# Performance work log

Hardware: AMD Instinct MI355X
Metric: run time of the kernel (lower is better)

## Reference

```python
import jax, jax.numpy as jnp
import numpy as np

B, H, W, C, HEADS = 4, 64, 64, 512, 8
HD = C // HEADS
L = H * W
BIAS_LEVEL = 0.1
LN_EPS = 1e-5


def _ln(x, g, b):
    mu = jnp.mean(x, axis=-1, keepdims=True)
    var = jnp.var(x, axis=-1, keepdims=True)
    return (x - mu) * jax.lax.rsqrt(var + LN_EPS) * g + b


def setup_inputs() -> dict:
    key = jax.random.key(0)
    ks = jax.random.split(key, 16)
    s = 0.02
    return {
        "x": jax.random.normal(ks[0], (B, L, C), jnp.float32),
        "rpe": jax.random.normal(ks[1], (H, HEADS, W, W), jnp.float32),
        "qkv_w": jax.random.normal(ks[2], (3 * C, C), jnp.float32) * s,
        "proj_w": jax.random.normal(ks[3], (C, C), jnp.float32) * s,
        "proj_b": jnp.zeros((C,), jnp.float32),
        "norm1_w": jnp.ones((C,), jnp.float32),
        "norm1_b": jnp.zeros((C,), jnp.float32),
        "norm2_w": jnp.ones((C,), jnp.float32),
        "norm2_b": jnp.zeros((C,), jnp.float32),
        "fc1_w": jax.random.normal(ks[4], (4 * C, C), jnp.float32) * s,
        "fc1_b": jnp.zeros((4 * C,), jnp.float32),
        "fc2_w": jax.random.normal(ks[5], (C, 4 * C), jnp.float32) * s,
        "fc2_b": jnp.zeros((C,), jnp.float32),
    }


def reference(x, rpe, qkv_w, proj_w, proj_b, norm1_w, norm1_b, norm2_w, norm2_b,
              fc1_w, fc1_b, fc2_w, fc2_b):
    # --- qkv projection ---
    img = _ln(x, norm1_w, norm1_b)
    qkv = (img @ qkv_w.T).reshape(B, L, 3, C)
    q, k, v = qkv[:, :, 0], qkv[:, :, 1], qkv[:, :, 2]

    # idx=0 horizontal windows: each row of the HxW grid is a window of len W.
    def to_win(t):  # (B, L, C) -> (B*H, heads, W, hd)
        return t.reshape(B * H, W, HEADS, HD).transpose(0, 2, 1, 3)

    qw, kw, vw = to_win(q), to_win(k), to_win(v)

    # attention scores + relative position bias (RPE tiled over batch)
    attn = jnp.einsum('whqd,whkd->whqk', qw, kw)
    attn = attn + BIAS_LEVEL * jnp.tile(rpe, (B, 1, 1, 1))

    # magnitude gate M per window
    M = jnp.mean(jnp.abs(attn), axis=(1, 2, 3), keepdims=True)  # (B*H,1,1,1)
    M = M / jnp.max(M)
    M = jnp.maximum(M, 0.5)

    # cosine-based score transform: 1 - cos(pi/2 * l2normalize(attn))
    nrm = jnp.maximum(jnp.linalg.norm(attn, axis=-1, keepdims=True), 1e-12)
    attn = 1.0 - jnp.cos((attn / nrm) * (jnp.pi / 2.0))
    attn = attn * M

    o = jnp.einsum('whqk,whkd->whqd', attn, vw)  # (B*H, heads, W, hd)
    o = o.transpose(0, 2, 1, 3).reshape(B, L, C)

    # residual gating by (1 - M)
    res = (x.reshape(B * H, 1, W, C) * (1.0 - M)).reshape(B, L, C)
    attened = o + res

    attened = attened @ proj_w.T + proj_b
    x1 = x + attened

    h = _ln(x1, norm2_w, norm2_b)
    h = jax.nn.gelu(h @ fc1_w.T + fc1_b, approximate=False)
    h = h @ fc2_w.T + fc2_b
    return x1 + h
```

## Files before the change

kernel.cpp:

```cpp
#include <hip/hip_runtime.h>
#include <hip/hip_bf16.h>
#include <math.h>

typedef unsigned short u16;
typedef __bf16 bf16x8 __attribute__((ext_vector_type(8)));
typedef float f32x4 __attribute__((ext_vector_type(4)));
typedef unsigned short u16x8 __attribute__((ext_vector_type(8)));

typedef const __attribute__((address_space(1))) void* gas_ptr;
typedef __attribute__((address_space(3))) void* las_ptr;

__device__ __forceinline__ float bf2f(u16 u) {
    union { unsigned int i; float f; } x;
    x.i = ((unsigned int)u) << 16;
    return x.f;
}
__device__ __forceinline__ u16 f2bf(float f) {
    __hip_bfloat16 h = __float2bfloat16(f);
    return __builtin_bit_cast(u16, h);
}
__device__ __forceinline__ __bf16 f2bfr(float f) {
    __hip_bfloat16 h = __float2bfloat16(f);
    return __builtin_bit_cast(__bf16, h);
}
__device__ __forceinline__ void load_lds16(const void* g, void* l) {
    __builtin_amdgcn_global_load_lds((gas_ptr)g, (las_ptr)l, 16, 0, 0);
}
__device__ __forceinline__ float gelu_f(float v) {
    const float a = fabsf(v) * 0.70710678118654752f;
    const float tt = 1.0f / fmaf(0.3275911f, a, 1.0f);
    float poly = fmaf(tt, 1.061405429f, -1.453152027f);
    poly = fmaf(tt, poly, 1.421413741f);
    poly = fmaf(tt, poly, -0.284496736f);
    poly = fmaf(tt, poly, 0.254829592f);
    const float erfa = 1.0f - poly * tt * __expf(-a * a);
    const float erfv = copysignf(erfa, v);
    return 0.5f * v * (1.0f + erfv);
}

__global__ __launch_bounds__(256) void cvt_all_k(const float* __restrict__ qkv_w,
                                                 const float* __restrict__ proj_w,
                                                 const float* __restrict__ fc1w,
                                                 const float* __restrict__ fc2w,
                                                 u16* __restrict__ wqkv,
                                                 u16* __restrict__ wproj,
                                                 u16* __restrict__ wfc1,
                                                 u16* __restrict__ wfc2) {
    const int b = blockIdx.x;
    const float* src; u16* dst; int off;
    if (b < 768)       { src = qkv_w;  dst = wqkv;  off = b; }
    else if (b < 1024) { src = proj_w; dst = wproj; off = b - 768; }
    else if (b < 2048) { src = fc1w;   dst = wfc1;  off = b - 1024; }
    else               { src = fc2w;   dst = wfc2;  off = b - 2048; }
    const int i = off * 256 + threadIdx.x;
    const float4 v = ((const float4*)src)[i];
    ushort4 o;
    o.x = f2bf(v.x); o.y = f2bf(v.y); o.z = f2bf(v.z); o.w = f2bf(v.w);
    ((ushort4*)dst)[i] = o;
}

template<bool BF16IN>
__global__ __launch_bounds__(256) void ln_k(const void* __restrict__ inp,
                                            const float* __restrict__ gw,
                                            const float* __restrict__ gb,
                                            u16* __restrict__ outp) {
    const int row = blockIdx.x, t = threadIdx.x;
    float v0, v1;
    if (BF16IN) {
        const u16* rp = (const u16*)inp + (size_t)row * 512;
        v0 = bf2f(rp[2 * t]); v1 = bf2f(rp[2 * t + 1]);
    } else {
        const float2 v = ((const float2*)((const float*)inp + (size_t)row * 512))[t];
        v0 = v.x; v1 = v.y;
    }
    float s = v0 + v1, q = v0 * v0 + v1 * v1;
    #pragma unroll
    for (int o = 1; o < 64; o <<= 1) {
        s += __shfl_xor(s, o);
        q += __shfl_xor(q, o);
    }
    __shared__ float rs[4], rq[4];
    const int w = t >> 6;
    if ((t & 63) == 0) { rs[w] = s; rq[w] = q; }
    __syncthreads();
    s = rs[0] + rs[1] + rs[2] + rs[3];
    q = rq[0] + rq[1] + rq[2] + rq[3];
    const float mean = s * (1.0f / 512.0f);
    const float var = q * (1.0f / 512.0f) - mean * mean;
    const float rstd = rsqrtf(var + 1e-5f);
    u16* op = outp + (size_t)row * 512;
    op[2 * t]     = f2bf((v0 - mean) * rstd * gw[2 * t]     + gb[2 * t]);
    op[2 * t + 1] = f2bf((v1 - mean) * rstd * gw[2 * t + 1] + gb[2 * t + 1]);
}

template<int EPI, bool AFUSE>
__global__ __launch_bounds__(256) void gemm_bt(const u16* __restrict__ A,
                                               const u16* __restrict__ W,
                                               const float* __restrict__ bias,
                                               const float* __restrict__ res_f,
                                               const u16* __restrict__ res_bf,
                                               void* __restrict__ outp,
                                               int M, int N, int K,
                                               const float* __restrict__ aM,
                                               const u16* __restrict__ aO,
                                               const float* __restrict__ aX) {
    __shared__ __bf16 As[2][128 * 64];
    __shared__ __bf16 Bs[2][128 * 64];
    const int t = threadIdx.x;
    const int l = t & 63;
    const int w = t >> 6;
    const int wm = w & 1, wn = w >> 1;
    const int bm = blockIdx.x * 128, bn = blockIdx.y * 128;
    const int r = l & 15, g4 = l >> 4;

    f32x4 acc[4][4] = {};

    const int rowS = t >> 3;
    const int cS = (t & 7) ^ (rowS & 7);
    const size_t rstep = (size_t)32 * K;
    const u16* wBase = W + (size_t)(bn + rowS) * K + cS * 8;
    const u16* aBase = AFUSE ? nullptr : (A + (size_t)(bm + rowS) * K + cS * 8);
    const size_t afBase = (size_t)(bm + rowS) * K + cS * 8;

    auto stage = [&](int buf, int kt) {
        #pragma unroll
        for (int j = 0; j < 4; ++j) {
            if (AFUSE) {
                const size_t gidx = afBase + j * rstep + kt;
                const float Mw = aM[(bm + rowS + j * 32) >> 6];
                const float rf = 1.0f - Mw;
                const u16x8 ov = *(const u16x8*)(aO + gidx);
                const float4 x0 = *(const float4*)(aX + gidx);
                const float4 x1 = *(const float4*)(aX + gidx + 4);
                bf16x8 val;
                val[0] = f2bfr(Mw * bf2f(ov[0]) + rf * x0.x);
                val[1] = f2bfr(Mw * bf2f(ov[1]) + rf * x0.y);
                val[2] = f2bfr(Mw * bf2f(ov[2]) + rf * x0.z);
                val[3] = f2bfr(Mw * bf2f(ov[3]) + rf * x0.w);
                val[4] = f2bfr(Mw * bf2f(ov[4]) + rf * x1.x);
                val[5] = f2bfr(Mw * bf2f(ov[5]) + rf * x1.y);
                val[6] = f2bfr(Mw * bf2f(ov[6]) + rf * x1.z);
                val[7] = f2bfr(Mw * bf2f(ov[7]) + rf * x1.w);
                *(bf16x8*)&As[buf][(j * 256 + t) * 8] = val;
            } else {
                load_lds16(aBase + j * rstep + kt, &As[buf][(j * 256 + t) * 8]);
            }
            load_lds16(wBase + j * rstep + kt, &Bs[buf][(j * 256 + t) * 8]);
        }
    };

    const int nk = K >> 6;
    stage(0, 0);
    __syncthreads();
    for (int s = 0; s < nk; ++s) {
        if (s + 1 < nk) stage((s + 1) & 1, (s + 1) << 6);
        const int buf = s & 1;
        bf16x8 af[4][2], bfr[4][2];
        #pragma unroll
        for (int i = 0; i < 4; ++i) {
            const int ra = wm * 64 + i * 16 + r;
            const int rb = wn * 64 + i * 16 + r;
            #pragma unroll
            for (int h = 0; h < 2; ++h) {
                af[i][h]  = *(const bf16x8*)&As[buf][ra * 64 + (((h * 4 + g4) ^ (ra & 7)) << 3)];
                bfr[i][h] = *(const bf16x8*)&Bs[buf][rb * 64 + (((h * 4 + g4) ^ (rb & 7)) << 3)];
            }
        }
        #pragma unroll
        for (int i = 0; i < 4; ++i)
            #pragma unroll
            for (int j = 0; j < 4; ++j)
                #pragma unroll
                for (int h = 0; h < 2; ++h)
                    acc[i][j] = __builtin_amdgcn_mfma_f32_16x16x32_bf16(
                        af[i][h], bfr[j][h], acc[i][j], 0, 0, 0);
        __syncthreads();
    }

    #pragma unroll
    for (int i = 0; i < 4; ++i) {
        #pragma unroll
        for (int j = 0; j < 4; ++j) {
            #pragma unroll
            for (int rr = 0; rr < 4; ++rr) {
                const int m = bm + wm * 64 + i * 16 + g4 * 4 + rr;
                const int n = bn + wn * 64 + j * 16 + r;
                float v = acc[i][j][rr];
                const size_t idx = (size_t)m * N + n;
                if (EPI == 0) {
                    ((u16*)outp)[idx] = f2bf(v);
                } else if (EPI == 1) {
                    ((u16*)outp)[idx] = f2bf(v + bias[n] + res_f[idx]);
                } else if (EPI == 2) {
                    ((u16*)outp)[idx] = f2bf(gelu_f(v + bias[n]));
                } else {
                    ((float*)outp)[idx] = v + bias[n] + bf2f(res_bf[idx]);
                }
            }
        }
    }
}

__global__ __launch_bounds__(256) void attn_k(const u16* __restrict__ qkv,
                                              const float* __restrict__ rpe,
                                              float* __restrict__ Mpart,
                                              u16* __restrict__ Obuf) {
    const int blk = blockIdx.x;
    const int wh = blk >> 3, head = blk & 7;
    const int himg = wh & 63;
    const int t = threadIdx.x, l = t & 63, w = t >> 6;
    __shared__ __bf16 Qs[4096];
    __shared__ __bf16 Ks[4096];
    __shared__ __bf16 Vt[4096];
    __shared__ __bf16 Ps[4096];
    __shared__ float red[4];

    #pragma unroll
    for (int p = 0; p < 2; ++p) {
        const int sb = (p * 256 + t) << 4;
        const int row = sb >> 7;
        const int gl = ((sb >> 4) & 7) ^ (row & 7);
        const size_t gsrc = (size_t)(wh * 64 + row) * 1536 + head * 64 + gl * 8;
        const int lbase = p * 2048 + w * 512;
        load_lds16(qkv + gsrc, &Qs[lbase]);
        load_lds16(qkv + gsrc + 512, &Ks[lbase]);
    }
    {
        const int k = t >> 2, dc = (t & 3) * 16;
        const u16* vr = qkv + (size_t)(wh * 64 + k) * 1536 + 1024 + head * 64 + dc;
        u16x8 v0 = *(const u16x8*)vr;
        u16x8 v1 = *(const u16x8*)(vr + 8);
        const int g = k >> 3, klo = k & 7;
        #pragma unroll
        for (int i = 0; i < 8; ++i) {
            const int d0 = dc + i, d1 = dc + 8 + i;
            Vt[d0 * 64 + ((g ^ (d0 & 7)) << 3) + klo] = __builtin_bit_cast(__bf16, (u16)v0[i]);
            Vt[d1 * 64 + ((g ^ (d1 & 7)) << 3) + klo] = __builtin_bit_cast(__bf16, (u16)v1[i]);
        }
    }
    __syncthreads();

    const int r = l & 15, g4 = l >> 4;
    f32x4 acc[4] = {};
    #pragma unroll
    for (int h = 0; h < 2; ++h) {
        const int rowq = w * 16 + r;
        bf16x8 aq = *(const bf16x8*)&Qs[rowq * 64 + (((h * 4 + g4) ^ (rowq & 7)) << 3)];
        #pragma unroll
        for (int j = 0; j < 4; ++j) {
            const int rowk = j * 16 + r;
            bf16x8 bk = *(const bf16x8*)&Ks[rowk * 64 + (((h * 4 + g4) ^ (rowk & 7)) << 3)];
            acc[j] = __builtin_amdgcn_mfma_f32_16x16x32_bf16(aq, bk, acc[j], 0, 0, 0);
        }
    }

    float v[4][4];
    float asum = 0.f;
    float ss[4] = {0.f, 0.f, 0.f, 0.f};
    const size_t rpe_base = (size_t)(himg * 8 + head) * 4096 + (size_t)(w * 16 + g4 * 4) * 64 + r;
    #pragma unroll
    for (int j = 0; j < 4; ++j) {
        #pragma unroll
        for (int rr = 0; rr < 4; ++rr) {
            const float val = acc[j][rr] + 0.1f * rpe[rpe_base + rr * 64 + j * 16];
            v[j][rr] = val;
            asum += fabsf(val);
            ss[rr] += val * val;
        }
    }
    #pragma unroll
    for (int m = 1; m < 16; m <<= 1) {
        #pragma unroll
        for (int rr = 0; rr < 4; ++rr) ss[rr] += __shfl_xor(ss[rr], m);
    }
    float srev[4];
    #pragma unroll
    for (int rr = 0; rr < 4; ++rr)
        srev[rr] = 0.25f / fmaxf(sqrtf(ss[rr]), 1e-12f);

    #pragma unroll
    for (int j = 0; j < 4; ++j) {
        #pragma unroll
        for (int rr = 0; rr < 4; ++rr) {
            const float pv = 1.0f - __builtin_amdgcn_cosf(v[j][rr] * srev[rr]);
            const int rl = g4 * 4 + rr;
            const int c = j * 16 + r;
            Ps[w * 1024 + rl * 64 + (((c >> 3) ^ (rl & 7)) << 3) + (c & 7)] = f2bfr(pv);
        }
    }

    f32x4 oacc[4] = {};
    #pragma unroll
    for (int ks = 0; ks < 2; ++ks) {
        const int ga = ks * 4 + g4;
        bf16x8 pa = *(const bf16x8*)&Ps[w * 1024 + r * 64 + ((ga ^ (r & 7)) << 3)];
        #pragma unroll
        for (int j = 0; j < 4; ++j) {
            const int d = j * 16 + r;
            bf16x8 vb = *(const bf16x8*)&Vt[d * 64 + ((ga ^ (d & 7)) << 3)];
            oacc[j] = __builtin_amdgcn_mfma_f32_16x16x32_bf16(pa, vb, oacc[j], 0, 0, 0);
        }
    }

    #pragma unroll
    for (int j = 0; j < 4; ++j) {
        #pragma unroll
        for (int rr = 0; rr < 4; ++rr) {
            const int token = wh * 64 + w * 16 + g4 * 4 + rr;
            Obuf[(size_t)token * 512 + head * 64 + j * 16 + r] = f2bf(oacc[j][rr]);
        }
    }

    #pragma unroll
    for (int o = 1; o < 64; o <<= 1) asum += __shfl_xor(asum, o);
    if (l == 0) red[w] = asum;
    __syncthreads();
    if (t == 0) Mpart[blk] = red[0] + red[1] + red[2] + red[3];
}

__global__ __launch_bounds__(256) void mfinal_k(const float* __restrict__ Mpart,
                                                float* __restrict__ M) {
    const int t = threadIdx.x;
    float m = 0.f;
    #pragma unroll
    for (int h = 0; h < 8; ++h) m += Mpart[t * 8 + h];
    m *= (1.0f / 32768.0f);
    float mx = m;
    #pragma unroll
    for (int o = 1; o < 64; o <<= 1) mx = fmaxf(mx, __shfl_xor(mx, o));
    __shared__ float red[4];
    if ((t & 63) == 0) red[t >> 6] = mx;
    __syncthreads();
    mx = fmaxf(fmaxf(red[0], red[1]), fmaxf(red[2], red[3]));
    M[t] = fmaxf(m / mx, 0.5f);
}

extern "C" void kernel_launch(void* const* d_in, const int* in_sizes, int n_in,
                              void* d_out, int out_size, void* d_ws, size_t ws_size,
                              hipStream_t stream) {
    (void)in_sizes; (void)n_in; (void)out_size; (void)ws_size;
    const float* x      = (const float*)d_in[0];
    const float* rpe    = (const float*)d_in[1];
    const float* qkv_w  = (const float*)d_in[2];
    const float* proj_w = (const float*)d_in[3];
    const float* proj_b = (const float*)d_in[4];
    const float* n1w    = (const float*)d_in[5];
    const float* n1b    = (const float*)d_in[6];
    const float* n2w    = (const float*)d_in[7];
    const float* n2b    = (const float*)d_in[8];
    const float* fc1w   = (const float*)d_in[9];
    const float* fc1b   = (const float*)d_in[10];
    const float* fc2w   = (const float*)d_in[11];
    const float* fc2b   = (const float*)d_in[12];
    float* out = (float*)d_out;

    char* ws = (char*)d_ws;
    float* Mpart = (float*)ws;
    float* Mbuf  = (float*)(ws + 8192);
    u16* wqkv  = (u16*)(ws + 16384);
    u16* wproj = (u16*)(ws + 16384 + 1572864);
    u16* wfc1  = (u16*)(ws + 16384 + 2097152);
    u16* wfc2  = (u16*)(ws + 16384 + 4194304);
    u16* bufA  = (u16*)(ws + 6307840);
    u16* bufB  = (u16*)(ws + 23085056);
    char* R    = ws + 39862272;
    u16*   qkvb = (u16*)R;
    u16*   Obuf = (u16*)(R + 50331648);
    u16*   gbuf = (u16*)R;

    cvt_all_k<<<3072, 256, 0, stream>>>(qkv_w, proj_w, fc1w, fc2w,
                                        wqkv, wproj, wfc1, wfc2);
    ln_k<false><<<16384, 256, 0, stream>>>(x, n1w, n1b, bufA);
    gemm_bt<0, false><<<dim3(128, 12), 256, 0, stream>>>(
        bufA, wqkv, nullptr, nullptr, nullptr, qkvb, 16384, 1536, 512,
        nullptr, nullptr, nullptr);
    attn_k<<<2048, 256, 0, stream>>>(qkvb, rpe, Mpart, Obuf);
    mfinal_k<<<1, 256, 0, stream>>>(Mpart, Mbuf);
    gemm_bt<1, true><<<dim3(128, 4), 256, 0, stream>>>(
        nullptr, wproj, proj_b, x, nullptr, bufA, 16384, 512, 512,
        Mbuf, Obuf, x);
    ln_k<true><<<16384, 256, 0, stream>>>(bufA, n2w, n2b, bufB);
    gemm_bt<2, false><<<dim3(128, 16), 256, 0, stream>>>(
        bufB, wfc1, fc1b, nullptr, nullptr, gbuf, 16384, 2048, 512,
        nullptr, nullptr, nullptr);
    gemm_bt<3, false><<<dim3(128, 4), 256, 0, stream>>>(
        gbuf, wfc2, fc2b, nullptr, bufA, out, 16384, 512, 2048,
        nullptr, nullptr, nullptr);
}
```

Before: 198.3 us.

## Rework GEMM mainloop into triple-buffered BK=32 pipeline with fine-grained waits

The bf16 GEMM moves from a double-buffered K-tile of 64 to a three-stage ring of K-tile 32. It uses explicit vmcnt waits plus raw s_barrier instead of __syncthreads, so loads for stage s+2 stay in flight while stage s computes. It also swizzles LDS for the 32-wide rows and raises wave priority around the MFMA block. The intent is to hide global-to-LDS latency and cut barrier stalls, at the cost of more loop iterations and hand-managed waitcnt correctness.

```diff
diff --git a/kernel.cpp b/kernel.cpp
--- a/kernel.cpp
+++ b/kernel.cpp
@@ -25,6 +25,11 @@
 }
 __device__ __forceinline__ void load_lds16(const void* g, void* l) {
     __builtin_amdgcn_global_load_lds((gas_ptr)g, (las_ptr)l, 16, 0, 0);
+}
+__device__ __forceinline__ void phase_bar() {
+    __builtin_amdgcn_sched_barrier(0);
+    __builtin_amdgcn_s_barrier();
+    __builtin_amdgcn_sched_barrier(0);
 }
 __device__ __forceinline__ float gelu_f(float v) {
     const float a = fabsf(v) * 0.70710678118654752f;
@@ -104,8 +109,8 @@
                                                const float* __restrict__ aM,
                                                const u16* __restrict__ aO,
                                                const float* __restrict__ aX) {
-    __shared__ __bf16 As[2][128 * 64];
-    __shared__ __bf16 Bs[2][128 * 64];
+    __shared__ __bf16 As[3][128 * 32];
+    __shared__ __bf16 Bs[3][128 * 32];
     const int t = threadIdx.x;
     const int l = t & 63;
     const int w = t >> 6;
@@ -115,67 +120,88 @@
 
     f32x4 acc[4][4] = {};
 
-    const int rowS = t >> 3;
-    const int cS = (t & 7) ^ (rowS & 7);
-    const size_t rstep = (size_t)32 * K;
-    const u16* wBase = W + (size_t)(bn + rowS) * K + cS * 8;
-    const u16* aBase = AFUSE ? nullptr : (A + (size_t)(bm + rowS) * K + cS * 8);
-    const size_t afBase = (size_t)(bm + rowS) * K + cS * 8;
-
-    auto stage = [&](int buf, int kt) {
-        #pragma unroll
-        for (int j = 0; j < 4; ++j) {
-            if (AFUSE) {
-                const size_t gidx = afBase + j * rstep + kt;
-                const float Mw = aM[(bm + rowS + j * 32) >> 6];
-                const float rf = 1.0f - Mw;
-                const u16x8 ov = *(const u16x8*)(aO + gidx);
-                const float4 x0 = *(const float4*)(aX + gidx);
-                const float4 x1 = *(const float4*)(aX + gidx + 4);
-                bf16x8 val;
-                val[0] = f2bfr(Mw * bf2f(ov[0]) + rf * x0.x);
-                val[1] = f2bfr(Mw * bf2f(ov[1]) + rf * x0.y);
-                val[2] = f2bfr(Mw * bf2f(ov[2]) + rf * x0.z);
-                val[3] = f2bfr(Mw * bf2f(ov[3]) + rf * x0.w);
-                val[4] = f2bfr(Mw * bf2f(ov[4]) + rf * x1.x);
-                val[5] = f2bfr(Mw * bf2f(ov[5]) + rf * x1.y);
-                val[6] = f2bfr(Mw * bf2f(ov[6]) + rf * x1.z);
-                val[7] = f2bfr(Mw * bf2f(ov[7]) + rf * x1.w);
-                *(bf16x8*)&As[buf][(j * 256 + t) * 8] = val;
-            } else {
-                load_lds16(aBase + j * rstep + kt, &As[buf][(j * 256 + t) * 8]);
-            }
-            load_lds16(wBase + j * rstep + kt, &Bs[buf][(j * 256 + t) * 8]);
-        }
+    const int rowS0 = t >> 2, rowS1 = rowS0 + 64;
+    const int c0 = (t & 3) ^ ((rowS0 >> 1) & 3);
+    const int c1 = (t & 3) ^ ((rowS1 >> 1) & 3);
+    const u16* wB0 = W + (size_t)(bn + rowS0) * K + c0 * 8;
+    const u16* wB1 = W + (size_t)(bn + rowS1) * K + c1 * 8;
+    const u16* aB0 = A + (size_t)(bm + rowS0) * K + c0 * 8;
+    const u16* aB1 = A + (size_t)(bm + rowS1) * K + c1 * 8;
+    const float Mw0 = AFUSE ? aM[(bm + rowS0) >> 6] : 0.f;
+    const float Mw1 = AFUSE ? aM[(bm + rowS1) >> 6] : 0.f;
+
+    auto afuse_val = [&](const u16* oP, const float* xP, float Mw) {
+        const float rf = 1.0f - Mw;
+        const u16x8 ov = *(const u16x8*)oP;
+        const float4 x0 = *(const float4*)xP;
+        const float4 x1 = *(const float4*)(xP + 4);
+        bf16x8 val;
+        val[0] = f2bfr(Mw * bf2f(ov[0]) + rf * x0.x);
+        val[1] = f2bfr(Mw * bf2f(ov[1]) + rf * x0.y);
+        val[2] = f2bfr(Mw * bf2f(ov[2]) + rf * x0.z);
+        val[3] = f2bfr(Mw * bf2f(ov[3]) + rf * x0.w);
+        val[4] = f2bfr(Mw * bf2f(ov[4]) + rf * x1.x);
+        val[5] = f2bfr(Mw * bf2f(ov[5]) + rf * x1.y);
+        val[6] = f2bfr(Mw * bf2f(ov[6]) + rf * x1.z);
+        val[7] = f2bfr(Mw * bf2f(ov[7]) + rf * x1.w);
+        return val;
     };
 
-    const int nk = K >> 6;
-    stage(0, 0);
-    __syncthreads();
-    for (int s = 0; s < nk; ++s) {
-        if (s + 1 < nk) stage((s + 1) & 1, (s + 1) << 6);
-        const int buf = s & 1;
-        bf16x8 af[4][2], bfr[4][2];
+    auto stage = [&](int buf, int kt) __attribute__((always_inline)) {
+        load_lds16(wB0 + kt, &Bs[buf][w * 512]);
+        load_lds16(wB1 + kt, &Bs[buf][2048 + w * 512]);
+        if (AFUSE) {
+            const size_t g0 = (size_t)(bm + rowS0) * K + c0 * 8 + kt;
+            const size_t g1 = (size_t)(bm + rowS1) * K + c1 * 8 + kt;
+            *(bf16x8*)&As[buf][t * 8]       = afuse_val(aO + g0, aX + g0, Mw0);
+            *(bf16x8*)&As[buf][2048 + t * 8] = afuse_val(aO + g1, aX + g1, Mw1);
+        } else {
+            load_lds16(aB0 + kt, &As[buf][w * 512]);
+            load_lds16(aB1 + kt, &As[buf][2048 + w * 512]);
+        }
+    };
+
+    auto compute = [&](int buf) __attribute__((always_inline)) {
+        bf16x8 af[4], bfr[4];
         #pragma unroll
         for (int i = 0; i < 4; ++i) {
             const int ra = wm * 64 + i * 16 + r;
+            af[i] = *(const bf16x8*)&As[buf][ra * 32 + ((g4 ^ ((ra >> 1) & 3)) << 3)];
             const int rb = wn * 64 + i * 16 + r;
-            #pragma unroll
-            for (int h = 0; h < 2; ++h) {
-                af[i][h]  = *(const bf16x8*)&As[buf][ra * 64 + (((h * 4 + g4) ^ (ra & 7)) << 3)];
-                bfr[i][h] = *(const bf16x8*)&Bs[buf][rb * 64 + (((h * 4 + g4) ^ (rb & 7)) << 3)];
-            }
-        }
+            bfr[i] = *(const bf16x8*)&Bs[buf][rb * 32 + ((g4 ^ ((rb >> 1) & 3)) << 3)];
+        }
+        __builtin_amdgcn_s_setprio(1);
         #pragma unroll
         for (int i = 0; i < 4; ++i)
             #pragma unroll
             for (int j = 0; j < 4; ++j)
-                #pragma unroll
-                for (int h = 0; h < 2; ++h)
-                    acc[i][j] = __builtin_amdgcn_mfma_f32_16x16x32_bf16(
-                        af[i][h], bfr[j][h], acc[i][j], 0, 0, 0);
-        __syncthreads();
-    }
+                acc[i][j] = __builtin_amdgcn_mfma_f32_16x16x32_bf16(
+                    af[i], bfr[j], acc[i][j], 0, 0, 0);
+        __builtin_amdgcn_s_setprio(0);
+    };
+
+    const int nk = K >> 5;
+    stage(0, 0);
+    stage(1, 32);
+    if (AFUSE) asm volatile("s_waitcnt vmcnt(0) lgkmcnt(0)" ::: "memory");
+    else       asm volatile("s_waitcnt vmcnt(4)" ::: "memory");
+    phase_bar();
+
+    int bc = 0;
+    for (int s = 0; s < nk - 2; ++s) {
+        const int bs = bc + 2 >= 3 ? bc - 1 : bc + 2;
+        stage(bs, (s + 2) << 5);
+        compute(bc);
+        if (AFUSE) asm volatile("s_waitcnt vmcnt(0) lgkmcnt(0)" ::: "memory");
+        else       asm volatile("s_waitcnt vmcnt(4)" ::: "memory");
+        phase_bar();
+        bc = bc + 1 >= 3 ? 0 : bc + 1;
+    }
+    compute(bc);
+    asm volatile("s_waitcnt vmcnt(0) lgkmcnt(0)" ::: "memory");
+    phase_bar();
+    bc = bc + 1 >= 3 ? 0 : bc + 1;
+    compute(bc);
 
     #pragma unroll
     for (int i = 0; i < 4; ++i) {
@@ -377,7 +403,7 @@
     attn_k<<<2048, 256, 0, stream>>>(qkvb, rpe, Mpart, Obuf);
     mfinal_k<<<1, 256, 0, stream>>>(Mpart, Mbuf);
     gemm_bt<1, true><<<dim3(128, 4), 256, 0, stream>>>(
-        nullptr, wproj, proj_b, x, nullptr, bufA, 16384, 512, 512,
+        Obuf, wproj, proj_b, x, nullptr, bufA, 16384, 512, 512,
         Mbuf, Obuf, x);
     ln_k<true><<<16384, 256, 0, stream>>>(bufA, n2w, n2b, bufB);
     gemm_bt<2, false><<<dim3(128, 16), 256, 0, stream>>>(
```

Result: slower. 225.0 us (+13.5%).

## Fuse LayerNorm2 into proj epilogue stats and fc1 A-operand staging

Applied to the files above, without the earlier changes.

The proj GEMM epilogue now emits per-row partial sum and sum-of-squares, a tiny kernel reduces them to mean/rstd, and the fc1 GEMM normalizes its bf16 A tiles on the fly while staging into LDS. This removes the standalone LN2 kernel and its extra bf16 write and read of the activation. LN1 is rewritten to one wave per row with vectorized float4 loads and 16-byte stores, and the M gate values are hoisted out of the staging loop. In exchange, fc1 staging goes through registers instead of direct-to-LDS loads, and it redoes the normalization in every one of the 16 N-tile blocks. Statistics are also computed from unrounded fp32 values while the normalized input is the rounded bf16.

```diff
diff --git a/kernel.cpp b/kernel.cpp
--- a/kernel.cpp
+++ b/kernel.cpp
@@ -59,41 +59,55 @@
     ((ushort4*)dst)[i] = o;
 }
 
-template<bool BF16IN>
-__global__ __launch_bounds__(256) void ln_k(const void* __restrict__ inp,
-                                            const float* __restrict__ gw,
-                                            const float* __restrict__ gb,
-                                            u16* __restrict__ outp) {
-    const int row = blockIdx.x, t = threadIdx.x;
-    float v0, v1;
-    if (BF16IN) {
-        const u16* rp = (const u16*)inp + (size_t)row * 512;
-        v0 = bf2f(rp[2 * t]); v1 = bf2f(rp[2 * t + 1]);
-    } else {
-        const float2 v = ((const float2*)((const float*)inp + (size_t)row * 512))[t];
-        v0 = v.x; v1 = v.y;
-    }
-    float s = v0 + v1, q = v0 * v0 + v1 * v1;
+__global__ __launch_bounds__(256) void ln_row_k(const float* __restrict__ x,
+                                                const float* __restrict__ gw,
+                                                const float* __restrict__ gb,
+                                                u16* __restrict__ outp) {
+    const int row = blockIdx.x * 4 + (threadIdx.x >> 6);
+    const int lane = threadIdx.x & 63;
+    const float* rp = x + (size_t)row * 512 + lane * 8;
+    const float4 a = *(const float4*)rp;
+    const float4 b = *(const float4*)(rp + 4);
+    float s = a.x + a.y + a.z + a.w + b.x + b.y + b.z + b.w;
+    float q = a.x*a.x + a.y*a.y + a.z*a.z + a.w*a.w
+            + b.x*b.x + b.y*b.y + b.z*b.z + b.w*b.w;
     #pragma unroll
     for (int o = 1; o < 64; o <<= 1) {
         s += __shfl_xor(s, o);
         q += __shfl_xor(q, o);
     }
-    __shared__ float rs[4], rq[4];
-    const int w = t >> 6;
-    if ((t & 63) == 0) { rs[w] = s; rq[w] = q; }
-    __syncthreads();
-    s = rs[0] + rs[1] + rs[2] + rs[3];
-    q = rq[0] + rq[1] + rq[2] + rq[3];
     const float mean = s * (1.0f / 512.0f);
     const float var = q * (1.0f / 512.0f) - mean * mean;
     const float rstd = rsqrtf(var + 1e-5f);
-    u16* op = outp + (size_t)row * 512;
-    op[2 * t]     = f2bf((v0 - mean) * rstd * gw[2 * t]     + gb[2 * t]);
-    op[2 * t + 1] = f2bf((v1 - mean) * rstd * gw[2 * t + 1] + gb[2 * t + 1]);
-}
-
-template<int EPI, bool AFUSE>
+    const float4 g0 = *(const float4*)(gw + lane * 8);
+    const float4 g1 = *(const float4*)(gw + lane * 8 + 4);
+    const float4 c0 = *(const float4*)(gb + lane * 8);
+    const float4 c1 = *(const float4*)(gb + lane * 8 + 4);
+    u16x8 o16;
+    o16[0] = f2bf((a.x - mean) * rstd * g0.x + c0.x);
+    o16[1] = f2bf((a.y - mean) * rstd * g0.y + c0.y);
+    o16[2] = f2bf((a.z - mean) * rstd * g0.z + c0.z);
+    o16[3] = f2bf((a.w - mean) * rstd * g0.w + c0.w);
+    o16[4] = f2bf((b.x - mean) * rstd * g1.x + c1.x);
+    o16[5] = f2bf((b.y - mean) * rstd * g1.y + c1.y);
+    o16[6] = f2bf((b.z - mean) * rstd * g1.z + c1.z);
+    o16[7] = f2bf((b.w - mean) * rstd * g1.w + c1.w);
+    *(u16x8*)(outp + (size_t)row * 512 + lane * 8) = o16;
+}
+
+__global__ __launch_bounds__(256) void ln2stat_k(const float* __restrict__ statP,
+                                                 float* __restrict__ lnst) {
+    const int row = blockIdx.x * 256 + threadIdx.x;
+    const float4* p = (const float4*)(statP + (size_t)row * 16);
+    const float4 a = p[0], b = p[1], c = p[2], d = p[3];
+    const float s = a.x + a.z + b.x + b.z + c.x + c.z + d.x + d.z;
+    const float q = a.y + a.w + b.y + b.w + c.y + c.w + d.y + d.w;
+    const float mean = s * (1.0f / 512.0f);
+    const float var = q * (1.0f / 512.0f) - mean * mean;
+    ((float2*)lnst)[row] = make_float2(mean, rsqrtf(var + 1e-5f));
+}
+
+template<int EPI, int AFUSE>
 __global__ __launch_bounds__(256) void gemm_bt(const u16* __restrict__ A,
                                                const u16* __restrict__ W,
                                                const float* __restrict__ bias,
@@ -103,7 +117,11 @@
                                                int M, int N, int K,
                                                const float* __restrict__ aM,
                                                const u16* __restrict__ aO,
-                                               const float* __restrict__ aX) {
+                                               const float* __restrict__ aX,
+                                               float* __restrict__ statP,
+                                               const float* __restrict__ lnst,
+                                               const float* __restrict__ lngw,
+                                               const float* __restrict__ lngb) {
     __shared__ __bf16 As[2][128 * 64];
     __shared__ __bf16 Bs[2][128 * 64];
     const int t = threadIdx.x;
@@ -119,28 +137,55 @@
     const int cS = (t & 7) ^ (rowS & 7);
     const size_t rstep = (size_t)32 * K;
     const u16* wBase = W + (size_t)(bn + rowS) * K + cS * 8;
-    const u16* aBase = AFUSE ? nullptr : (A + (size_t)(bm + rowS) * K + cS * 8);
+    const u16* aBase = A + (size_t)(bm + rowS) * K + cS * 8;
     const size_t afBase = (size_t)(bm + rowS) * K + cS * 8;
 
+    float Mw[4], lnmean[4], lnrstd[4];
+    if (AFUSE == 1) {
+        #pragma unroll
+        for (int j = 0; j < 4; ++j) Mw[j] = aM[(bm + rowS + 32 * j) >> 6];
+    } else if (AFUSE == 2) {
+        #pragma unroll
+        for (int j = 0; j < 4; ++j) {
+            const float2 st = ((const float2*)lnst)[bm + rowS + 32 * j];
+            lnmean[j] = st.x; lnrstd[j] = st.y;
+        }
+    }
+
     auto stage = [&](int buf, int kt) {
+        float gwv[8], gbv[8];
+        if (AFUSE == 2) {
+            const int kc = kt + cS * 8;
+            *(float4*)&gwv[0] = *(const float4*)(lngw + kc);
+            *(float4*)&gwv[4] = *(const float4*)(lngw + kc + 4);
+            *(float4*)&gbv[0] = *(const float4*)(lngb + kc);
+            *(float4*)&gbv[4] = *(const float4*)(lngb + kc + 4);
+        }
         #pragma unroll
         for (int j = 0; j < 4; ++j) {
-            if (AFUSE) {
+            if (AFUSE == 1) {
                 const size_t gidx = afBase + j * rstep + kt;
-                const float Mw = aM[(bm + rowS + j * 32) >> 6];
-                const float rf = 1.0f - Mw;
+                const float rf = 1.0f - Mw[j];
                 const u16x8 ov = *(const u16x8*)(aO + gidx);
                 const float4 x0 = *(const float4*)(aX + gidx);
                 const float4 x1 = *(const float4*)(aX + gidx + 4);
                 bf16x8 val;
-                val[0] = f2bfr(Mw * bf2f(ov[0]) + rf * x0.x);
-                val[1] = f2bfr(Mw * bf2f(ov[1]) + rf * x0.y);
-                val[2] = f2bfr(Mw * bf2f(ov[2]) + rf * x0.z);
-                val[3] = f2bfr(Mw * bf2f(ov[3]) + rf * x0.w);
-                val[4] = f2bfr(Mw * bf2f(ov[4]) + rf * x1.x);
-                val[5] = f2bfr(Mw * bf2f(ov[5]) + rf * x1.y);
-                val[6] = f2bfr(Mw * bf2f(ov[6]) + rf * x1.z);
-                val[7] = f2bfr(Mw * bf2f(ov[7]) + rf * x1.w);
+                val[0] = f2bfr(Mw[j] * bf2f(ov[0]) + rf * x0.x);
+                val[1] = f2bfr(Mw[j] * bf2f(ov[1]) + rf * x0.y);
+                val[2] = f2bfr(Mw[j] * bf2f(ov[2]) + rf * x0.z);
+                val[3] = f2bfr(Mw[j] * bf2f(ov[3]) + rf * x0.w);
+                val[4] = f2bfr(Mw[j] * bf2f(ov[4]) + rf * x1.x);
+                val[5] = f2bfr(Mw[j] * bf2f(ov[5]) + rf * x1.y);
+                val[6] = f2bfr(Mw[j] * bf2f(ov[6]) + rf * x1.z);
+                val[7] = f2bfr(Mw[j] * bf2f(ov[7]) + rf * x1.w);
+                *(bf16x8*)&As[buf][(j * 256 + t) * 8] = val;
+            } else if (AFUSE == 2) {
+                const size_t gidx = afBase + j * rstep + kt;
+                const u16x8 xv = *(const u16x8*)(A + gidx);
+                bf16x8 val;
+                #pragma unroll
+                for (int e = 0; e < 8; ++e)
+                    val[e] = f2bfr((bf2f(xv[e]) - lnmean[j]) * lnrstd[j] * gwv[e] + gbv[e]);
                 *(bf16x8*)&As[buf][(j * 256 + t) * 8] = val;
             } else {
                 load_lds16(aBase + j * rstep + kt, &As[buf][(j * 256 + t) * 8]);
@@ -180,22 +225,35 @@
     #pragma unroll
     for (int i = 0; i < 4; ++i) {
         #pragma unroll
-        for (int j = 0; j < 4; ++j) {
+        for (int rr = 0; rr < 4; ++rr) {
+            const int m = bm + wm * 64 + i * 16 + g4 * 4 + rr;
+            float s = 0.f, q = 0.f;
             #pragma unroll
-            for (int rr = 0; rr < 4; ++rr) {
-                const int m = bm + wm * 64 + i * 16 + g4 * 4 + rr;
+            for (int j = 0; j < 4; ++j) {
                 const int n = bn + wn * 64 + j * 16 + r;
                 float v = acc[i][j][rr];
                 const size_t idx = (size_t)m * N + n;
                 if (EPI == 0) {
                     ((u16*)outp)[idx] = f2bf(v);
                 } else if (EPI == 1) {
-                    ((u16*)outp)[idx] = f2bf(v + bias[n] + res_f[idx]);
+                    v += bias[n] + res_f[idx];
+                    ((u16*)outp)[idx] = f2bf(v);
+                    s += v; q += v * v;
                 } else if (EPI == 2) {
                     ((u16*)outp)[idx] = f2bf(gelu_f(v + bias[n]));
                 } else {
                     ((float*)outp)[idx] = v + bias[n] + bf2f(res_bf[idx]);
                 }
+            }
+            if (EPI == 1) {
+                #pragma unroll
+                for (int o = 1; o < 16; o <<= 1) {
+                    s += __shfl_xor(s, o);
+                    q += __shfl_xor(q, o);
+                }
+                if (r == 0)
+                    ((float2*)statP)[(size_t)m * 8 + blockIdx.y * 2 + wn] =
+                        make_float2(s, q);
             }
         }
     }
@@ -362,7 +420,8 @@
     u16* wfc1  = (u16*)(ws + 16384 + 2097152);
     u16* wfc2  = (u16*)(ws + 16384 + 4194304);
     u16* bufA  = (u16*)(ws + 6307840);
-    u16* bufB  = (u16*)(ws + 23085056);
+    float* statP = (float*)(ws + 23085056);
+    float* lnst  = (float*)(ws + 23085056 + 1048576);
     char* R    = ws + 39862272;
     u16*   qkvb = (u16*)R;
     u16*   Obuf = (u16*)(R + 50331648);
@@ -370,20 +429,20 @@
 
     cvt_all_k<<<3072, 256, 0, stream>>>(qkv_w, proj_w, fc1w, fc2w,
                                         wqkv, wproj, wfc1, wfc2);
-    ln_k<false><<<16384, 256, 0, stream>>>(x, n1w, n1b, bufA);
-    gemm_bt<0, false><<<dim3(128, 12), 256, 0, stream>>>(
+    ln_row_k<<<4096, 256, 0, stream>>>(x, n1w, n1b, bufA);
+    gemm_bt<0, 0><<<dim3(128, 12), 256, 0, stream>>>(
         bufA, wqkv, nullptr, nullptr, nullptr, qkvb, 16384, 1536, 512,
-        nullptr, nullptr, nullptr);
+        nullptr, nullptr, nullptr, nullptr, nullptr, nullptr, nullptr);
     attn_k<<<2048, 256, 0, stream>>>(qkvb, rpe, Mpart, Obuf);
     mfinal_k<<<1, 256, 0, stream>>>(Mpart, Mbuf);
-    gemm_bt<1, true><<<dim3(128, 4), 256, 0, stream>>>(
-        nullptr, wproj, proj_b, x, nullptr, bufA, 16384, 512, 512,
-        Mbuf, Obuf, x);
-    ln_k<true><<<16384, 256, 0, stream>>>(bufA, n2w, n2b, bufB);
-    gemm_bt<2, false><<<dim3(128, 16), 256, 0, stream>>>(
-        bufB, wfc1, fc1b, nullptr, nullptr, gbuf, 16384, 2048, 512,
-        nullptr, nullptr, nullptr);
-    gemm_bt<3, false><<<dim3(128, 4), 256, 0, stream>>>(
+    gemm_bt<1, 1><<<dim3(128, 4), 256, 0, stream>>>(
+        Obuf, wproj, proj_b, x, nullptr, bufA, 16384, 512, 512,
+        Mbuf, Obuf, x, statP, nullptr, nullptr, nullptr);
+    ln2stat_k<<<64, 256, 0, stream>>>(statP, lnst);
+    gemm_bt<2, 2><<<dim3(128, 16), 256, 0, stream>>>(
+        bufA, wfc1, fc1b, nullptr, nullptr, gbuf, 16384, 2048, 512,
+        nullptr, nullptr, nullptr, nullptr, lnst, n2w, n2b);
+    gemm_bt<3, 0><<<dim3(128, 4), 256, 0, stream>>>(
         gbuf, wfc2, fc2b, nullptr, bufA, out, 16384, 512, 2048,
-        nullptr, nullptr, nullptr);
-}
+        nullptr, nullptr, nullptr, nullptr, nullptr, nullptr, nullptr);
+}
```

After: 206.6 us. +4.1%, slower.
